# Kernel optimization log

Hardware: AMD Instinct MI355X
Metric: run time of the kernel (lower is better)

## Reference

```python
import jax, jax.numpy as jnp
import numpy as np

BS, SEQ, D_IN, D_OUT = 4, 1024, 1024, 1024
N_SKILLS, RANK = 8, 4
SCALING = 1.0  # lora_alpha / rank, folded into one constant
NEG_INF = -1e38


def setup_inputs() -> dict:
    key = jax.random.key(0)
    ks = jax.random.split(key, 5)
    x = jax.random.normal(ks[0], (BS, SEQ, D_IN), jnp.float32)
    phi = jax.random.normal(ks[1], (D_IN, N_SKILLS), jnp.float32) * 0.02
    lora_a = jax.random.normal(ks[2], (N_SKILLS, D_IN, RANK), jnp.float32) * 0.02
    lora_b = jax.random.normal(ks[3], (N_SKILLS, RANK, D_OUT), jnp.float32) * 0.02
    W = jax.random.normal(ks[4], (D_OUT, D_IN), jnp.float32) * 0.02
    b = jnp.zeros((D_OUT,), jnp.float32)
    # left-padded sequences with an instruction prefix right after the padding
    pad_len = np.array([100, 0, 250, 50])
    inst_len = 300
    pad = np.zeros((BS, SEQ), np.int32)
    inst = np.zeros((BS, SEQ), np.int32)
    for i in range(BS):
        pad[i, pad_len[i]:] = 1
        inst[i, pad_len[i]:pad_len[i] + inst_len] = 1
    return {"x": x, "phi": phi, "lora_a": lora_a, "lora_b": lora_b,
            "W": W, "b": b,
            "inst_mask": jnp.asarray(inst), "pad_mask": jnp.asarray(pad)}


def _causal_prefix_mask(inst_mask, pad_mask):
    # faithful port of create_causal_prefix_mask (padding_side='left')
    bs, seq = inst_mask.shape
    first_one = jnp.argmax(inst_mask, axis=1, keepdims=True)          # [b,1]
    n_ones = jnp.sum(inst_mask, axis=1, keepdims=True)                # [b,1]
    thresh = first_one + n_ones                                       # last_one_idx + 1
    exp = jnp.broadcast_to(thresh, (bs, seq))                         # [b,s]
    inv = jnp.maximum(seq - exp - jnp.arange(seq)[None, :], 0)[:, ::-1]
    m = (exp + inv) * pad_mask                                        # [b,s]
    m3 = m[:, :, None] * pad_mask[:, None, :]                         # [b,s,s]
    ar = jnp.arange(seq)[None, None, :]
    return ar < m3                                                    # bool [b,s,s]


def reference(x, phi, lora_a, lora_b, W, b, inst_mask, pad_mask):
    # router: mixing logits per token per skill
    mw = jnp.einsum('bsd,dn->bsn', x, phi)                            # [b,s,k]
    cm = _causal_prefix_mask(inst_mask, pad_mask)                     # [b,s,s]
    padf = pad_mask.astype(x.dtype)
    # expand over attended positions p, mask, softmax over p
    logits = jnp.where(cm[..., None], mw[:, :, None, :], NEG_INF)     # [b,s,p,k]
    logits = jnp.transpose(logits, (0, 3, 1, 2))                      # [b,k,s,p]
    D = jax.nn.softmax(logits, axis=-1)
    D = D * padf[:, None, :, None]                                    # zero padded query rows
    # token mixing: contract over source tokens (last axis of D)
    input_mixed = jnp.einsum('bsd,bkps->bkpd', x, D)                  # [b,k,s,d]
    # per-skill LoRA (n_splits == 1, q squeezed)
    ar_r = jnp.einsum('bksd,kdr->bskr', input_mixed, lora_a)          # [b,s,k,r]
    ad = jnp.einsum('bskr,krd->bskd', ar_r, lora_b)                   # [b,s,k,d_out]
    # softmax-weighted combine over skills
    C = jax.nn.softmax(mw, axis=-1)
    adapter_out = jnp.einsum('bsk,bskd->bsd', C, ad) * SCALING
    base = jnp.einsum('bsd,od->bso', x, W) + b
    return base + adapter_out
```

## Files before the change

kernel.cpp:

```cpp
#include <hip/hip_runtime.h>
#include <hip/hip_bf16.h>
#include <cstdint>

#define SEQ   1024
#define DOUT  1024
#define KDIM  1024
#define MTOT  4096
#define WCROWS 1072

typedef __bf16 bf16x8 __attribute__((ext_vector_type(8)));
typedef float  f32x4  __attribute__((ext_vector_type(4)));

__device__ inline unsigned short f2bf(float f) {
  union { float f; unsigned u; } a; a.f = f;
  unsigned r = a.u + 0x7fff + ((a.u >> 16) & 1);
  return (unsigned short)(r >> 16);
}

__device__ inline void gl16(const void* g, void* l) {
  __builtin_amdgcn_global_load_lds((__attribute__((address_space(1))) void*)g,
                                   (__attribute__((address_space(3))) void*)l, 16, 0, 0);
}

__global__ __launch_bounds__(256) void k_prep(const float4* __restrict__ x, ushort4* __restrict__ xb,
                                              const float* __restrict__ W, const float* __restrict__ phi,
                                              const float* __restrict__ la, const float* __restrict__ lb,
                                              unsigned short* __restrict__ Wc, unsigned short* __restrict__ B2T,
                                              const int* __restrict__ inst, int* __restrict__ thr) {
  int blk = blockIdx.x, tid = threadIdx.x;
  if (blk < 4096) {
    int i = blk * 256 + tid;
    float4 v = x[i];
    ushort4 o; o.x = f2bf(v.x); o.y = f2bf(v.y); o.z = f2bf(v.z); o.w = f2bf(v.w);
    xb[i] = o;
  } else if (blk < 8384) {
    int i = (blk - 4096) * 256 + tid;
    int row = i >> 10, d = i & 1023;
    float v;
    if (row < 1024)       v = W[i];
    else if (row < 1032)  v = phi[d * 8 + (row - 1024)];
    else if (row < 1064)  { int kr = row - 1032; v = la[(kr >> 2) * 4096 + d * 4 + (kr & 3)]; }
    else                  v = 0.f;
    Wc[i] = f2bf(v);
  } else if (blk < 8512) {
    int i = (blk - 8384) * 256 + tid;
    int n = i >> 5, kr = i & 31;
    B2T[i] = f2bf(lb[kr * 1024 + n]);
  } else {
    int b = tid >> 6, lane = tid & 63;
    int fo = 1 << 30, no = 0;
#pragma unroll
    for (int j = 0; j < 16; ++j) {
      int p = j * 64 + lane;
      int iv = inst[b * SEQ + p];
      if (iv > 0) fo = min(fo, p);
      no += iv;
    }
#pragma unroll
    for (int d = 1; d < 64; d <<= 1) { fo = min(fo, __shfl_xor(fo, d)); no += __shfl_xor(no, d); }
    if (lane == 0) thr[b] = (no > 0) ? fo + no : 0;
  }
}

__global__ __launch_bounds__(256) void k_mwz(const unsigned short* __restrict__ xb,
                                             const unsigned short* __restrict__ Wc,
                                             float* __restrict__ mwzP) {
  __shared__ unsigned short As[2][64 * 32];
  __shared__ unsigned short Bs[2][48 * 32];
  int bm = blockIdx.x, ks = blockIdx.y;
  int t = threadIdx.x, wave = t >> 6, lane = t & 63;
  int quad = lane >> 4, lr = lane & 15;
  f32x4 acc[3];
#pragma unroll
  for (int i = 0; i < 3; ++i) acc[i] = (f32x4){0.f, 0.f, 0.f, 0.f};
  const unsigned short* aG = xb + (size_t)bm * 64 * KDIM + ks * 256;
  const unsigned short* bG = Wc + (size_t)1024 * KDIM + ks * 256;
  int r0 = t >> 2, c0 = (t & 3) * 8;

#define MWZ_STAGE(i) { int buf_ = (i) & 1; int kb_ = (i) * 32;                         \
    gl16(aG + (size_t)r0 * KDIM + kb_ + c0, &As[buf_][wave * 512]);                    \
    if (wave < 3) gl16(bG + (size_t)r0 * KDIM + kb_ + c0, &Bs[buf_][wave * 512]); }

  MWZ_STAGE(0)
  for (int i = 0; i < 8; ++i) {
    __syncthreads();
    if (i < 7) MWZ_STAGE(i + 1)
    int buf = i & 1;
    bf16x8 af = *(const bf16x8*)&As[buf][(wave * 16 + lr) * 32 + quad * 8];
#pragma unroll
    for (int ni = 0; ni < 3; ++ni) {
      bf16x8 bfr = *(const bf16x8*)&Bs[buf][(ni * 16 + lr) * 32 + quad * 8];
      acc[ni] = __builtin_amdgcn_mfma_f32_16x16x32_bf16(af, bfr, acc[ni], 0, 0, 0);
    }
  }
#pragma unroll
  for (int ni = 0; ni < 3; ++ni) {
    int c = ni * 16 + lr;
#pragma unroll
    for (int rg = 0; rg < 4; ++rg) {
      int row = bm * 64 + wave * 16 + quad * 4 + rg;
      if (c < 40) mwzP[(size_t)(ks * 40 + c) * MTOT + row] = acc[ni][rg];
    }
  }
}

__global__ __launch_bounds__(1024) void k_scan_gate(const float* __restrict__ mwzP,
                                                    const int* __restrict__ pad, const int* __restrict__ thr,
                                                    unsigned short* __restrict__ gb) {
  int b = blockIdx.x, c = blockIdx.y;
  int tid = threadIdx.x, wv = tid >> 6, lane = tid & 63;
  __shared__ float wsz[16], wsp[16];
  __shared__ float sv, spc;
  int q = b * SEQ + tid;
  float pm = (float)pad[q];
  float z = 0.f;
#pragma unroll
  for (int s = 0; s < 4; ++s) z += mwzP[(size_t)(s * 40 + 8 + c) * MTOT + q];
  z *= pm;
  float vz = z, vp = pm;
#pragma unroll
  for (int d = 1; d < 64; d <<= 1) {
    float oz = __shfl_up(vz, d), op = __shfl_up(vp, d);
    if (lane >= d) { vz += oz; vp += op; }
  }
  if (lane == 63) { wsz[wv] = vz; wsp[wv] = vp; }
  __syncthreads();
  if (wv == 0 && lane < 16) {
    float oz = wsz[lane], op = wsp[lane], sz = oz, sp = op;
#pragma unroll
    for (int d = 1; d < 16; d <<= 1) {
      float tz = __shfl_up(sz, d), tp = __shfl_up(sp, d);
      if (lane >= d) { sz += tz; sp += tp; }
    }
    wsz[lane] = sz - oz; wsp[lane] = sp - op;
  }
  __syncthreads();
  vz += wsz[wv]; vp += wsp[wv];
  int th = thr[b];
  if (th > 0 && tid == th - 1) { sv = vz; spc = vp; }
  __syncthreads();
  unsigned short o = 0;
  if (pm != 0.f) {
    bool own = (tid + 1 >= th);
    float Tv  = own ? vz : sv;
    float cnt = own ? vp : spc;
    float C[8], mx = -1e30f;
#pragma unroll
    for (int k = 0; k < 8; ++k) {
      float m = 0.f;
#pragma unroll
      for (int s = 0; s < 4; ++s) m += mwzP[(size_t)(s * 40 + k) * MTOT + q];
      C[k] = m; mx = fmaxf(mx, m);
    }
    float sm = 0.f;
#pragma unroll
    for (int k = 0; k < 8; ++k) { C[k] = __expf(C[k] - mx); sm += C[k]; }
    o = f2bf(C[c >> 2] * Tv / (sm * cnt));
  }
  gb[(size_t)q * 32 + c] = o;
}

__global__ __launch_bounds__(256) void k_gemm(const unsigned short* __restrict__ A,
                                              const unsigned short* __restrict__ Wc,
                                              const unsigned short* __restrict__ gb,
                                              const unsigned short* __restrict__ B2T,
                                              float* __restrict__ out,
                                              const float* __restrict__ bias) {
  __shared__ unsigned short As[2][128 * 32];
  __shared__ unsigned short Bs[2][64 * 32];
  int bm = blockIdx.x, bn = blockIdx.y;
  int t = threadIdx.x;
  int wave = t >> 6, lane = t & 63;
  int wr = wave >> 1, wc = wave & 1;
  int quad = lane >> 4, lr = lane & 15;
  f32x4 acc[4][2];
#pragma unroll
  for (int i = 0; i < 4; i++)
#pragma unroll
    for (int j = 0; j < 2; j++) acc[i][j] = (f32x4){0.f, 0.f, 0.f, 0.f};

  const unsigned short* aG = A + (size_t)bm * 128 * KDIM;
  const unsigned short* bG = Wc + (size_t)bn * 64 * KDIM;
  const unsigned short* gA = gb + (size_t)bm * 128 * 32;
  const unsigned short* gB = B2T + (size_t)bn * 64 * 32;
  int r0 = t >> 2, c0 = (t & 3) * 8;

#define GEMM_STAGE(i) { int buf_ = (i) & 1;                                            \
    if ((i) < 32) { int kb_ = (i) * 32;                                                \
      gl16(aG + (size_t)r0 * KDIM + kb_ + c0,        &As[buf_][wave * 512]);           \
      gl16(aG + (size_t)(r0 + 64) * KDIM + kb_ + c0, &As[buf_][2048 + wave * 512]);    \
      gl16(bG + (size_t)r0 * KDIM + kb_ + c0,        &Bs[buf_][wave * 512]);           \
    } else {                                                                           \
      gl16(gA + (size_t)r0 * 32 + c0,        &As[buf_][wave * 512]);                   \
      gl16(gA + (size_t)(r0 + 64) * 32 + c0, &As[buf_][2048 + wave * 512]);            \
      gl16(gB + (size_t)r0 * 32 + c0,        &Bs[buf_][wave * 512]);                   \
    } }

  GEMM_STAGE(0)
  for (int i = 0; i < 33; ++i) {
    __syncthreads();
    if (i < 32) GEMM_STAGE(i + 1)
    int buf = i & 1;
    bf16x8 af[4], bfr[2];
#pragma unroll
    for (int mi = 0; mi < 4; mi++) af[mi]  = *(const bf16x8*)&As[buf][(wr * 64 + mi * 16 + lr) * 32 + quad * 8];
#pragma unroll
    for (int ni = 0; ni < 2; ni++) bfr[ni] = *(const bf16x8*)&Bs[buf][(wc * 32 + ni * 16 + lr) * 32 + quad * 8];
#pragma unroll
    for (int mi = 0; mi < 4; mi++)
#pragma unroll
      for (int ni = 0; ni < 2; ni++)
        acc[mi][ni] = __builtin_amdgcn_mfma_f32_16x16x32_bf16(af[mi], bfr[ni], acc[mi][ni], 0, 0, 0);
  }

#pragma unroll
  for (int mi = 0; mi < 4; mi++) {
#pragma unroll
    for (int ni = 0; ni < 2; ni++) {
      int col = bn * 64 + wc * 32 + ni * 16 + lr;
      float bv = bias[col];
#pragma unroll
      for (int rg = 0; rg < 4; ++rg) {
        int row = bm * 128 + wr * 64 + mi * 16 + quad * 4 + rg;
        out[(size_t)row * DOUT + col] = acc[mi][ni][rg] + bv;
      }
    }
  }
}

extern "C" void kernel_launch(void* const* d_in, const int* in_sizes, int n_in,
                              void* d_out, int out_size, void* d_ws, size_t ws_size,
                              hipStream_t stream) {
  const float* x    = (const float*)d_in[0];
  const float* phi  = (const float*)d_in[1];
  const float* la   = (const float*)d_in[2];
  const float* lb   = (const float*)d_in[3];
  const float* W    = (const float*)d_in[4];
  const float* bias = (const float*)d_in[5];
  const int*   inst = (const int*)d_in[6];
  const int*   pad  = (const int*)d_in[7];
  float* out = (float*)d_out;

  char* ws = (char*)d_ws;
  unsigned short* xb  = (unsigned short*)ws;
  unsigned short* Wc  = (unsigned short*)(ws + 8388608);
  unsigned short* B2T = (unsigned short*)(ws + 10584064);
  float* mwzP = (float*)(ws + 10649600);
  unsigned short* gb  = (unsigned short*)(ws + 13271040);
  int*   thr  = (int*)(ws + 13533184);

  hipLaunchKernelGGL(k_prep,      dim3(8513),   dim3(256),  0, stream,
                     (const float4*)x, (ushort4*)xb, W, phi, la, lb, Wc, B2T, inst, thr);
  hipLaunchKernelGGL(k_mwz,       dim3(64, 4),  dim3(256),  0, stream, xb, Wc, mwzP);
  hipLaunchKernelGGL(k_scan_gate, dim3(4, 32),  dim3(1024), 0, stream, mwzP, pad, thr, gb);
  hipLaunchKernelGGL(k_gemm,      dim3(32, 16), dim3(256),  0, stream, xb, Wc, gb, B2T, out, bias);
}
```

Baseline: 119.9 us.

## Fuse four kernels into one cooperative persistent kernel with grid syncs

Replaces the prep, router GEMM, scan-gate and main GEMM launches with a single cooperative kernel of 512 blocks that separates the phases with grid.sync. The aim is to remove kernel launch gaps and per-launch overhead. Along the way the GEMM loops drop their LDS double-buffering and go to single-buffered load/sync/compute. The scan is reworked to 256 threads, each handling 4 positions. The trade-offs are grid-wide barrier cost, less load/compute overlap in the main GEMM, and far fewer blocks in the prep phase (512 instead of 8513).

```diff
diff --git a/kernel.cpp b/kernel.cpp
--- a/kernel.cpp
+++ b/kernel.cpp
@@ -1,12 +1,16 @@
 #include <hip/hip_runtime.h>
 #include <hip/hip_bf16.h>
+#include <hip/hip_cooperative_groups.h>
 #include <cstdint>
+
+namespace cg = cooperative_groups;
 
 #define SEQ   1024
 #define DOUT  1024
 #define KDIM  1024
 #define MTOT  4096
 #define WCROWS 1072
+#define NBLK  512
 
 typedef __bf16 bf16x8 __attribute__((ext_vector_type(8)));
 typedef float  f32x4  __attribute__((ext_vector_type(4)));
@@ -22,19 +26,34 @@
                                    (__attribute__((address_space(3))) void*)l, 16, 0, 0);
 }
 
-__global__ __launch_bounds__(256) void k_prep(const float4* __restrict__ x, ushort4* __restrict__ xb,
-                                              const float* __restrict__ W, const float* __restrict__ phi,
-                                              const float* __restrict__ la, const float* __restrict__ lb,
-                                              unsigned short* __restrict__ Wc, unsigned short* __restrict__ B2T,
-                                              const int* __restrict__ inst, int* __restrict__ thr) {
+__global__ __launch_bounds__(256, 2) void k_fused(
+    const float4* __restrict__ x, ushort4* __restrict__ xb4,
+    const float* __restrict__ W, const float* __restrict__ phi,
+    const float* __restrict__ la, const float* __restrict__ lb,
+    unsigned short* __restrict__ Wc, unsigned short* __restrict__ B2T,
+    const int* __restrict__ inst, const int* __restrict__ pad, int* __restrict__ thr,
+    float* __restrict__ mwzP, unsigned short* __restrict__ gb,
+    float* __restrict__ out, const float* __restrict__ bias) {
+  cg::grid_group grid = cg::this_grid();
   int blk = blockIdx.x, tid = threadIdx.x;
-  if (blk < 4096) {
-    int i = blk * 256 + tid;
+  int wv = tid >> 6, lane = tid & 63;
+
+  __shared__ union {
+    struct { unsigned short As[128 * 32]; unsigned short Bs[64 * 32]; } g;
+    struct { unsigned short As[64 * 32];  unsigned short Bs[48 * 32]; } m;
+    struct { float pz[1024]; float pp[1024]; float wo[8]; } s;
+  } u;
+
+  const unsigned short* xb = (const unsigned short*)xb4;
+
+  for (int j = blk; j < 4096; j += NBLK) {
+    int i = j * 256 + tid;
     float4 v = x[i];
     ushort4 o; o.x = f2bf(v.x); o.y = f2bf(v.y); o.z = f2bf(v.z); o.w = f2bf(v.w);
-    xb[i] = o;
-  } else if (blk < 8384) {
-    int i = (blk - 4096) * 256 + tid;
+    xb4[i] = o;
+  }
+  for (int j = blk; j < 4288; j += NBLK) {
+    int i = j * 256 + tid;
     int row = i >> 10, d = i & 1023;
     float v;
     if (row < 1024)       v = W[i];
@@ -42,13 +61,14 @@
     else if (row < 1064)  { int kr = row - 1032; v = la[(kr >> 2) * 4096 + d * 4 + (kr & 3)]; }
     else                  v = 0.f;
     Wc[i] = f2bf(v);
-  } else if (blk < 8512) {
-    int i = (blk - 8384) * 256 + tid;
+  }
+  if (blk < 128) {
+    int i = blk * 256 + tid;
     int n = i >> 5, kr = i & 31;
     B2T[i] = f2bf(lb[kr * 1024 + n]);
-  } else {
-    int b = tid >> 6, lane = tid & 63;
-    int fo = 1 << 30, no = 0;
+  }
+  if (blk == 511) {
+    int b = wv, fo = 1 << 30, no = 0;
 #pragma unroll
     for (int j = 0; j < 16; ++j) {
       int p = j * 64 + lane;
@@ -60,169 +80,157 @@
     for (int d = 1; d < 64; d <<= 1) { fo = min(fo, __shfl_xor(fo, d)); no += __shfl_xor(no, d); }
     if (lane == 0) thr[b] = (no > 0) ? fo + no : 0;
   }
-}
-
-__global__ __launch_bounds__(256) void k_mwz(const unsigned short* __restrict__ xb,
-                                             const unsigned short* __restrict__ Wc,
-                                             float* __restrict__ mwzP) {
-  __shared__ unsigned short As[2][64 * 32];
-  __shared__ unsigned short Bs[2][48 * 32];
-  int bm = blockIdx.x, ks = blockIdx.y;
-  int t = threadIdx.x, wave = t >> 6, lane = t & 63;
-  int quad = lane >> 4, lr = lane & 15;
-  f32x4 acc[3];
-#pragma unroll
-  for (int i = 0; i < 3; ++i) acc[i] = (f32x4){0.f, 0.f, 0.f, 0.f};
-  const unsigned short* aG = xb + (size_t)bm * 64 * KDIM + ks * 256;
-  const unsigned short* bG = Wc + (size_t)1024 * KDIM + ks * 256;
-  int r0 = t >> 2, c0 = (t & 3) * 8;
-
-#define MWZ_STAGE(i) { int buf_ = (i) & 1; int kb_ = (i) * 32;                         \
-    gl16(aG + (size_t)r0 * KDIM + kb_ + c0, &As[buf_][wave * 512]);                    \
-    if (wave < 3) gl16(bG + (size_t)r0 * KDIM + kb_ + c0, &Bs[buf_][wave * 512]); }
-
-  MWZ_STAGE(0)
-  for (int i = 0; i < 8; ++i) {
+  __threadfence();
+  grid.sync();
+
+  if (blk < 256) {
+    int bm = blk >> 2, ks = blk & 3;
+    int quad = lane >> 4, lr = lane & 15;
+    f32x4 acc[3];
+#pragma unroll
+    for (int i = 0; i < 3; ++i) acc[i] = (f32x4){0.f, 0.f, 0.f, 0.f};
+    const unsigned short* aG = xb + (size_t)bm * 64 * KDIM + ks * 256;
+    const unsigned short* bG = Wc + (size_t)1024 * KDIM + ks * 256;
+    int r0 = tid >> 2, c0 = (tid & 3) * 8;
+    for (int kb = 0; kb < 256; kb += 32) {
+      __syncthreads();
+      gl16(aG + (size_t)r0 * KDIM + kb + c0, &u.m.As[wv * 512]);
+      if (wv < 3) gl16(bG + (size_t)r0 * KDIM + kb + c0, &u.m.Bs[wv * 512]);
+      __syncthreads();
+      bf16x8 af = *(const bf16x8*)&u.m.As[(wv * 16 + lr) * 32 + quad * 8];
+#pragma unroll
+      for (int ni = 0; ni < 3; ++ni) {
+        bf16x8 bfr = *(const bf16x8*)&u.m.Bs[(ni * 16 + lr) * 32 + quad * 8];
+        acc[ni] = __builtin_amdgcn_mfma_f32_16x16x32_bf16(af, bfr, acc[ni], 0, 0, 0);
+      }
+    }
+#pragma unroll
+    for (int ni = 0; ni < 3; ++ni) {
+      int c = ni * 16 + lr;
+#pragma unroll
+      for (int rg = 0; rg < 4; ++rg) {
+        int row = bm * 64 + wv * 16 + quad * 4 + rg;
+        if (c < 40) mwzP[(size_t)(ks * 40 + c) * MTOT + row] = acc[ni][rg];
+      }
+    }
+  }
+  __threadfence();
+  grid.sync();
+
+  if (blk < 128) {
+    int b = blk >> 5, c = blk & 31;
+    int t4 = tid * 4, q0 = b * SEQ + t4;
+    float zz[4], pm[4], lz[4], lp[4];
+#pragma unroll
+    for (int j = 0; j < 4; ++j) {
+      pm[j] = (float)pad[q0 + j];
+      float z = 0.f;
+#pragma unroll
+      for (int s = 0; s < 4; ++s) z += mwzP[(size_t)(s * 40 + 8 + c) * MTOT + q0 + j];
+      zz[j] = z * pm[j];
+    }
+    lz[0] = zz[0]; lp[0] = pm[0];
+#pragma unroll
+    for (int j = 1; j < 4; ++j) { lz[j] = lz[j-1] + zz[j]; lp[j] = lp[j-1] + pm[j]; }
+    float tz = lz[3], tp = lp[3], sz = tz, sp = tp;
+#pragma unroll
+    for (int d = 1; d < 64; d <<= 1) {
+      float oz = __shfl_up(sz, d), op = __shfl_up(sp, d);
+      if (lane >= d) { sz += oz; sp += op; }
+    }
+    float ez = sz - tz, ep = sp - tp;
+    if (lane == 63) { u.s.wo[wv] = sz; u.s.wo[4 + wv] = sp; }
     __syncthreads();
-    if (i < 7) MWZ_STAGE(i + 1)
-    int buf = i & 1;
-    bf16x8 af = *(const bf16x8*)&As[buf][(wave * 16 + lr) * 32 + quad * 8];
-#pragma unroll
-    for (int ni = 0; ni < 3; ++ni) {
-      bf16x8 bfr = *(const bf16x8*)&Bs[buf][(ni * 16 + lr) * 32 + quad * 8];
-      acc[ni] = __builtin_amdgcn_mfma_f32_16x16x32_bf16(af, bfr, acc[ni], 0, 0, 0);
-    }
-  }
-#pragma unroll
-  for (int ni = 0; ni < 3; ++ni) {
-    int c = ni * 16 + lr;
-#pragma unroll
-    for (int rg = 0; rg < 4; ++rg) {
-      int row = bm * 64 + wave * 16 + quad * 4 + rg;
-      if (c < 40) mwzP[(size_t)(ks * 40 + c) * MTOT + row] = acc[ni][rg];
-    }
-  }
-}
-
-__global__ __launch_bounds__(1024) void k_scan_gate(const float* __restrict__ mwzP,
-                                                    const int* __restrict__ pad, const int* __restrict__ thr,
-                                                    unsigned short* __restrict__ gb) {
-  int b = blockIdx.x, c = blockIdx.y;
-  int tid = threadIdx.x, wv = tid >> 6, lane = tid & 63;
-  __shared__ float wsz[16], wsp[16];
-  __shared__ float sv, spc;
-  int q = b * SEQ + tid;
-  float pm = (float)pad[q];
-  float z = 0.f;
-#pragma unroll
-  for (int s = 0; s < 4; ++s) z += mwzP[(size_t)(s * 40 + 8 + c) * MTOT + q];
-  z *= pm;
-  float vz = z, vp = pm;
-#pragma unroll
-  for (int d = 1; d < 64; d <<= 1) {
-    float oz = __shfl_up(vz, d), op = __shfl_up(vp, d);
-    if (lane >= d) { vz += oz; vp += op; }
-  }
-  if (lane == 63) { wsz[wv] = vz; wsp[wv] = vp; }
-  __syncthreads();
-  if (wv == 0 && lane < 16) {
-    float oz = wsz[lane], op = wsp[lane], sz = oz, sp = op;
-#pragma unroll
-    for (int d = 1; d < 16; d <<= 1) {
-      float tz = __shfl_up(sz, d), tp = __shfl_up(sp, d);
-      if (lane >= d) { sz += tz; sp += tp; }
-    }
-    wsz[lane] = sz - oz; wsp[lane] = sp - op;
-  }
-  __syncthreads();
-  vz += wsz[wv]; vp += wsp[wv];
-  int th = thr[b];
-  if (th > 0 && tid == th - 1) { sv = vz; spc = vp; }
-  __syncthreads();
-  unsigned short o = 0;
-  if (pm != 0.f) {
-    bool own = (tid + 1 >= th);
-    float Tv  = own ? vz : sv;
-    float cnt = own ? vp : spc;
-    float C[8], mx = -1e30f;
-#pragma unroll
-    for (int k = 0; k < 8; ++k) {
-      float m = 0.f;
-#pragma unroll
-      for (int s = 0; s < 4; ++s) m += mwzP[(size_t)(s * 40 + k) * MTOT + q];
-      C[k] = m; mx = fmaxf(mx, m);
-    }
-    float sm = 0.f;
-#pragma unroll
-    for (int k = 0; k < 8; ++k) { C[k] = __expf(C[k] - mx); sm += C[k]; }
-    o = f2bf(C[c >> 2] * Tv / (sm * cnt));
-  }
-  gb[(size_t)q * 32 + c] = o;
-}
-
-__global__ __launch_bounds__(256) void k_gemm(const unsigned short* __restrict__ A,
-                                              const unsigned short* __restrict__ Wc,
-                                              const unsigned short* __restrict__ gb,
-                                              const unsigned short* __restrict__ B2T,
-                                              float* __restrict__ out,
-                                              const float* __restrict__ bias) {
-  __shared__ unsigned short As[2][128 * 32];
-  __shared__ unsigned short Bs[2][64 * 32];
-  int bm = blockIdx.x, bn = blockIdx.y;
-  int t = threadIdx.x;
-  int wave = t >> 6, lane = t & 63;
-  int wr = wave >> 1, wc = wave & 1;
-  int quad = lane >> 4, lr = lane & 15;
-  f32x4 acc[4][2];
-#pragma unroll
-  for (int i = 0; i < 4; i++)
-#pragma unroll
-    for (int j = 0; j < 2; j++) acc[i][j] = (f32x4){0.f, 0.f, 0.f, 0.f};
-
-  const unsigned short* aG = A + (size_t)bm * 128 * KDIM;
-  const unsigned short* bG = Wc + (size_t)bn * 64 * KDIM;
-  const unsigned short* gA = gb + (size_t)bm * 128 * 32;
-  const unsigned short* gB = B2T + (size_t)bn * 64 * 32;
-  int r0 = t >> 2, c0 = (t & 3) * 8;
-
-#define GEMM_STAGE(i) { int buf_ = (i) & 1;                                            \
-    if ((i) < 32) { int kb_ = (i) * 32;                                                \
-      gl16(aG + (size_t)r0 * KDIM + kb_ + c0,        &As[buf_][wave * 512]);           \
-      gl16(aG + (size_t)(r0 + 64) * KDIM + kb_ + c0, &As[buf_][2048 + wave * 512]);    \
-      gl16(bG + (size_t)r0 * KDIM + kb_ + c0,        &Bs[buf_][wave * 512]);           \
-    } else {                                                                           \
-      gl16(gA + (size_t)r0 * 32 + c0,        &As[buf_][wave * 512]);                   \
-      gl16(gA + (size_t)(r0 + 64) * 32 + c0, &As[buf_][2048 + wave * 512]);            \
-      gl16(gB + (size_t)r0 * 32 + c0,        &Bs[buf_][wave * 512]);                   \
-    } }
-
-  GEMM_STAGE(0)
-  for (int i = 0; i < 33; ++i) {
+    float woz = 0.f, wop = 0.f;
+    for (int w = 0; w < wv; ++w) { woz += u.s.wo[w]; wop += u.s.wo[4 + w]; }
+#pragma unroll
+    for (int j = 0; j < 4; ++j) {
+      u.s.pz[t4 + j] = woz + ez + lz[j];
+      u.s.pp[t4 + j] = wop + ep + lp[j];
+    }
     __syncthreads();
-    if (i < 32) GEMM_STAGE(i + 1)
-    int buf = i & 1;
-    bf16x8 af[4], bfr[2];
-#pragma unroll
-    for (int mi = 0; mi < 4; mi++) af[mi]  = *(const bf16x8*)&As[buf][(wr * 64 + mi * 16 + lr) * 32 + quad * 8];
-#pragma unroll
-    for (int ni = 0; ni < 2; ni++) bfr[ni] = *(const bf16x8*)&Bs[buf][(wc * 32 + ni * 16 + lr) * 32 + quad * 8];
-#pragma unroll
-    for (int mi = 0; mi < 4; mi++)
-#pragma unroll
-      for (int ni = 0; ni < 2; ni++)
-        acc[mi][ni] = __builtin_amdgcn_mfma_f32_16x16x32_bf16(af[mi], bfr[ni], acc[mi][ni], 0, 0, 0);
-  }
-
-#pragma unroll
-  for (int mi = 0; mi < 4; mi++) {
-#pragma unroll
-    for (int ni = 0; ni < 2; ni++) {
-      int col = bn * 64 + wc * 32 + ni * 16 + lr;
-      float bv = bias[col];
-#pragma unroll
-      for (int rg = 0; rg < 4; ++rg) {
-        int row = bm * 128 + wr * 64 + mi * 16 + quad * 4 + rg;
-        out[(size_t)row * DOUT + col] = acc[mi][ni][rg] + bv;
+    int th = thr[b];
+    float sv = 0.f, spc = 1.f;
+    if (th > 0) { sv = u.s.pz[th - 1]; spc = u.s.pp[th - 1]; }
+#pragma unroll
+    for (int j = 0; j < 4; ++j) {
+      int s = t4 + j, q = q0 + j;
+      unsigned short o = 0;
+      if (pm[j] != 0.f) {
+        bool own = (s + 1 >= th);
+        float Tv  = own ? u.s.pz[s] : sv;
+        float cnt = own ? u.s.pp[s] : spc;
+        float C[8], mx = -1e30f;
+#pragma unroll
+        for (int k = 0; k < 8; ++k) {
+          float m = 0.f;
+#pragma unroll
+          for (int ss = 0; ss < 4; ++ss) m += mwzP[(size_t)(ss * 40 + k) * MTOT + q];
+          C[k] = m; mx = fmaxf(mx, m);
+        }
+        float sm = 0.f;
+#pragma unroll
+        for (int k = 0; k < 8; ++k) { C[k] = __expf(C[k] - mx); sm += C[k]; }
+        o = f2bf(C[c >> 2] * Tv / (sm * cnt));
+      }
+      gb[(size_t)q * 32 + c] = o;
+    }
+  }
+  __threadfence();
+  grid.sync();
+
+  {
+    int bm = blk & 31, bn = blk >> 5;
+    int wr = wv >> 1, wc = wv & 1;
+    int quad = lane >> 4, lr = lane & 15;
+    f32x4 acc[4][2];
+#pragma unroll
+    for (int i = 0; i < 4; i++)
+#pragma unroll
+      for (int j = 0; j < 2; j++) acc[i][j] = (f32x4){0.f, 0.f, 0.f, 0.f};
+
+    const unsigned short* aG = xb + (size_t)bm * 128 * KDIM;
+    const unsigned short* bG = Wc + (size_t)bn * 64 * KDIM;
+    const unsigned short* gA = gb + (size_t)bm * 128 * 32;
+    const unsigned short* gB = B2T + (size_t)bn * 64 * 32;
+    int r0 = tid >> 2, c0 = (tid & 3) * 8;
+
+    for (int i = 0; i < 33; ++i) {
+      __syncthreads();
+      if (i < 32) {
+        int kb = i * 32;
+        gl16(aG + (size_t)r0 * KDIM + kb + c0,        &u.g.As[wv * 512]);
+        gl16(aG + (size_t)(r0 + 64) * KDIM + kb + c0, &u.g.As[2048 + wv * 512]);
+        gl16(bG + (size_t)r0 * KDIM + kb + c0,        &u.g.Bs[wv * 512]);
+      } else {
+        gl16(gA + (size_t)r0 * 32 + c0,        &u.g.As[wv * 512]);
+        gl16(gA + (size_t)(r0 + 64) * 32 + c0, &u.g.As[2048 + wv * 512]);
+        gl16(gB + (size_t)r0 * 32 + c0,        &u.g.Bs[wv * 512]);
+      }
+      __syncthreads();
+      bf16x8 af[4], bfr[2];
+#pragma unroll
+      for (int mi = 0; mi < 4; mi++) af[mi]  = *(const bf16x8*)&u.g.As[(wr * 64 + mi * 16 + lr) * 32 + quad * 8];
+#pragma unroll
+      for (int ni = 0; ni < 2; ni++) bfr[ni] = *(const bf16x8*)&u.g.Bs[(wc * 32 + ni * 16 + lr) * 32 + quad * 8];
+#pragma unroll
+      for (int mi = 0; mi < 4; mi++)
+#pragma unroll
+        for (int ni = 0; ni < 2; ni++)
+          acc[mi][ni] = __builtin_amdgcn_mfma_f32_16x16x32_bf16(af[mi], bfr[ni], acc[mi][ni], 0, 0, 0);
+    }
+
+#pragma unroll
+    for (int mi = 0; mi < 4; mi++) {
+#pragma unroll
+      for (int ni = 0; ni < 2; ni++) {
+        int col = bn * 64 + wc * 32 + ni * 16 + lr;
+        float bv = bias[col];
+#pragma unroll
+        for (int rg = 0; rg < 4; ++rg) {
+          int row = bm * 128 + wr * 64 + mi * 16 + quad * 4 + rg;
+          out[(size_t)row * DOUT + col] = acc[mi][ni][rg] + bv;
+        }
       }
     }
   }
@@ -231,7 +239,7 @@
 extern "C" void kernel_launch(void* const* d_in, const int* in_sizes, int n_in,
                               void* d_out, int out_size, void* d_ws, size_t ws_size,
                               hipStream_t stream) {
-  const float* x    = (const float*)d_in[0];
+  const float4* x   = (const float4*)d_in[0];
   const float* phi  = (const float*)d_in[1];
   const float* la   = (const float*)d_in[2];
   const float* lb   = (const float*)d_in[3];
@@ -242,16 +250,15 @@
   float* out = (float*)d_out;
 
   char* ws = (char*)d_ws;
-  unsigned short* xb  = (unsigned short*)ws;
+  ushort4*        xb4 = (ushort4*)ws;
   unsigned short* Wc  = (unsigned short*)(ws + 8388608);
   unsigned short* B2T = (unsigned short*)(ws + 10584064);
   float* mwzP = (float*)(ws + 10649600);
   unsigned short* gb  = (unsigned short*)(ws + 13271040);
   int*   thr  = (int*)(ws + 13533184);
 
-  hipLaunchKernelGGL(k_prep,      dim3(8513),   dim3(256),  0, stream,
-                     (const float4*)x, (ushort4*)xb, W, phi, la, lb, Wc, B2T, inst, thr);
-  hipLaunchKernelGGL(k_mwz,       dim3(64, 4),  dim3(256),  0, stream, xb, Wc, mwzP);
-  hipLaunchKernelGGL(k_scan_gate, dim3(4, 32),  dim3(1024), 0, stream, mwzP, pad, thr, gb);
-  hipLaunchKernelGGL(k_gemm,      dim3(32, 16), dim3(256),  0, stream, xb, Wc, gb, B2T, out, bias);
-}
+  void* args[] = { (void*)&x, (void*)&xb4, (void*)&W, (void*)&phi, (void*)&la, (void*)&lb,
+                   (void*)&Wc, (void*)&B2T, (void*)&inst, (void*)&pad, (void*)&thr,
+                   (void*)&mwzP, (void*)&gb, (void*)&out, (void*)&bias };
+  hipLaunchCooperativeKernel((void*)k_fused, dim3(NBLK), dim3(256), args, 0, stream);
+}
```

Result: slower. 443.0 us (+269.4%).
